# Kernel optimization log

Hardware: AMD Instinct MI355X
Metric: run time of the kernel (lower is better)

The kernel has to match this reference:

```python
import jax, jax.numpy as jnp
import numpy as np

C = 256
R = 8
CR = C // R  # 32


def setup_inputs() -> dict:
    key = jax.random.key(0)
    kx, kq, kk, kv = jax.random.split(key, 4)
    x = jax.random.normal(kx, (4, C, 64, 64), dtype=jnp.float32)
    # 1x1 conv weights, no bias: [out_ch, in_ch]
    Wq = jax.random.normal(kq, (CR, C), dtype=jnp.float32) * (1.0 / np.sqrt(C))
    Wk = jax.random.normal(kk, (CR, C), dtype=jnp.float32) * (1.0 / np.sqrt(C))
    Wv = jax.random.normal(kv, (C, C), dtype=jnp.float32) * (1.0 / np.sqrt(C))
    return {"x": x, "Wq": Wq, "Wk": Wk, "Wv": Wv}


def reference(x, Wq, Wk, Wv):
    B, Cc, H, W = x.shape
    N = H * W
    xf = x.reshape(B, Cc, N)                      # [B, C, N]
    q = jnp.einsum('oc,bcn->bno', Wq, xf)         # [B, N, Cr]
    k = jnp.einsum('oc,bcn->bon', Wk, xf)         # [B, Cr, N]
    v = jnp.einsum('oc,bcn->bon', Wv, xf)         # [B, C, N]
    energy = jnp.einsum('bno,bom->bnm', q, k)     # [B, N, N]
    attn = jax.nn.softmax(energy, axis=-1)
    out = jnp.einsum('bcm,bnm->bcn', v, attn)     # [B, C, N]
    return out.reshape(B, Cc, H, W) + x
```

## Files before the change

kernel.cpp:

```cpp
#include <hip/hip_runtime.h>
#include <stdint.h>
#include <stddef.h>

#define Bn 4
#define Cn 256
#define CRn 32
#define Nn 4096

typedef __attribute__((ext_vector_type(8))) short short8v;
typedef __attribute__((ext_vector_type(4))) float f32x4;

__device__ __forceinline__ unsigned short f2bf(float f) {
  unsigned int u = __float_as_uint(f);
  u += 0x7FFFu + ((u >> 16) & 1u);
  return (unsigned short)(u >> 16);
}

__global__ void __launch_bounds__(256) k_wcast(const float* __restrict__ Wq,
                                               const float* __restrict__ Wk,
                                               const float* __restrict__ Wv,
                                               unsigned short* __restrict__ Wb) {
  int idx = (blockIdx.x * 256 + threadIdx.x) * 4;
  int row = idx >> 8, cc = idx & 255;
  const float* src = (row < 32) ? &Wq[row * 256 + cc]
                   : (row < 64) ? &Wk[(row - 32) * 256 + cc]
                                : &Wv[(row - 64) * 256 + cc];
  float4 f = *reinterpret_cast<const float4*>(src);
  ushort4 o;
  o.x = f2bf(f.x); o.y = f2bf(f.y); o.z = f2bf(f.z); o.w = f2bf(f.w);
  *reinterpret_cast<ushort4*>(&Wb[idx]) = o;
}

__global__ void __launch_bounds__(512) k_proj(const unsigned short* __restrict__ Wb,
                                              const float* __restrict__ x,
                                              unsigned short* __restrict__ Qt,
                                              unsigned short* __restrict__ Kt,
                                              unsigned short* __restrict__ V) {
  __shared__ __align__(16) unsigned char smem[54272];
  unsigned short* xs   = (unsigned short*)smem;
  unsigned short* wbuf = (unsigned short*)(smem + 33792);
  float*          xf   = (float*)(smem + 33792);
  unsigned short* vb   = (unsigned short*)smem;

  const int t  = threadIdx.x;
  const int nt = blockIdx.x, rt = blockIdx.y, b = blockIdx.z;
  const int rbase = rt * 160;
  const int li = t & 15, cr = t >> 4;

  for (int ct = 0; ct < 4; ++ct) {
    if (ct) __syncthreads();
#pragma unroll
    for (int p = 0; p < 2; ++p) {
      int c = cr + (p << 5);
      float4 f = *reinterpret_cast<const float4*>(
          &x[(((size_t)((b << 8) + (ct << 6) + c)) << 12) + (nt << 6) + (li << 2)]);
      xf[c * 65 + (li << 2) + 0] = f.x;
      xf[c * 65 + (li << 2) + 1] = f.y;
      xf[c * 65 + (li << 2) + 2] = f.z;
      xf[c * 65 + (li << 2) + 3] = f.w;
    }
    __syncthreads();
#pragma unroll
    for (int p = 0; p < 2; ++p) {
      int nl = cr + (p << 5);
      int cq = li << 2;
      ushort4 o;
      o.x = f2bf(xf[(cq + 0) * 65 + nl]);
      o.y = f2bf(xf[(cq + 1) * 65 + nl]);
      o.z = f2bf(xf[(cq + 2) * 65 + nl]);
      o.w = f2bf(xf[(cq + 3) * 65 + nl]);
      *reinterpret_cast<ushort4*>(&xs[nl * 264 + (ct << 6) + cq]) = o;
    }
  }
  __syncthreads();

  auto STAGEWB = [&](int ks, int buf) {
#pragma unroll
    for (int r = 0; r < 2; ++r) {
      int idx = (r << 9) + t;
      if (idx < 640) {
        int row = idx >> 2, seg = idx & 3;
        int sseg = seg ^ ((row ^ (row >> 2)) & 3);
        const unsigned short* g =
            Wb + (((size_t)(rbase + row)) << 8) + (ks << 5) + (sseg << 3);
        __builtin_amdgcn_global_load_lds(
            (const __attribute__((address_space(1))) void*)g,
            (__attribute__((address_space(3))) void*)(wbuf + buf * 5120 + idx * 8),
            16, 0, 0);
      }
    }
  };

  STAGEWB(0, 0);
  __syncthreads();

  const int lane = t & 63, w = t >> 6, col = lane & 15, hi = lane >> 4;
  const int nw = w & 3, rh2 = w >> 2;
  f32x4 zero4 = {0.f, 0.f, 0.f, 0.f};
  f32x4 acc[5];
#pragma unroll
  for (int rc = 0; rc < 5; ++rc) acc[rc] = zero4;

#pragma unroll 1
  for (int ks = 0; ks < 8; ++ks) {
    const unsigned short* wB = wbuf + (ks & 1) * 5120;
    if (ks < 7) STAGEWB(ks + 1, (ks & 1) ^ 1);
    short8v af = *reinterpret_cast<const short8v*>(
        &xs[((nw << 4) + col) * 264 + (ks << 5) + (hi << 3)]);
#pragma unroll
    for (int rc = 0; rc < 5; ++rc) {
      int row = rh2 * 80 + (rc << 4) + col;
      int sw = hi ^ ((row ^ (row >> 2)) & 3);
      short8v bf = *reinterpret_cast<const short8v*>(wB + row * 32 + (sw << 3));
      acc[rc] = __builtin_amdgcn_mfma_f32_16x16x32_bf16(af, bf, acc[rc], 0, 0, 0);
    }
    __syncthreads();
  }

  if (rt == 0 && rh2 == 0) {
#pragma unroll
    for (int rc = 0; rc < 2; ++rc)
#pragma unroll
      for (int r = 0; r < 4; ++r) {
        int n = (nt << 6) + (nw << 4) + (hi << 2) + r;
        Qt[(((size_t)((b << 12) + n)) << 5) + (rc << 4) + col] = f2bf(acc[rc][r]);
      }
#pragma unroll
    for (int rc = 2; rc < 4; ++rc)
#pragma unroll
      for (int r = 0; r < 4; ++r) {
        int n = (nt << 6) + (nw << 4) + (hi << 2) + r;
        Kt[(((size_t)((b << 12) + n)) << 5) + ((rc - 2) << 4) + col] = f2bf(acc[rc][r]);
      }
  }

  const int nch = rt ? 160 : 96;
  {
    const int nb = (nw << 4) + (hi << 2);
    const int sub = (rt == 0) ? 64 : 0;
#pragma unroll
    for (int rc = 0; rc < 5; ++rc) {
      int grow_l = rh2 * 80 + (rc << 4) + col;
      int ch_l = grow_l - sub;
      if (ch_l >= 0) {
#pragma unroll
        for (int r = 0; r < 4; ++r)
          vb[ch_l * 72 + nb + r] = f2bf(acc[rc][r]);
      }
    }
  }
  __syncthreads();

  const int cgBase = rt ? 96 : 0;
#pragma unroll
  for (int p = 0; p < 3; ++p) {
    int idx = (p << 9) + t;
    if (idx < nch * 8) {
      int c = idx >> 3, off = idx & 7;
      int offp = off ^ (c & 7);
      int4 dv = *reinterpret_cast<const int4*>(&vb[c * 72 + (offp << 3)]);
      *reinterpret_cast<int4*>(
          &V[(((size_t)((b << 8) + cgBase + c)) << 12) + (nt << 6) + (offp << 3)]) = dv;
    }
  }
}

__global__ void __launch_bounds__(512, 2) k_attn(const unsigned short* __restrict__ Qt,
                                                 const unsigned short* __restrict__ Kt,
                                                 const unsigned short* __restrict__ Vv,
                                                 const float* __restrict__ x,
                                                 float* __restrict__ out) {
  __shared__ unsigned short Qs[64][40];
  __shared__ __align__(16) unsigned short Pt[2][2][64 * 64];
  __shared__ float Sc[2][2][64];
  __shared__ float Mm[2][64], Ll[2][64];
  __shared__ float Ob[4][16][64];

  const int t = threadIdx.x, bx = blockIdx.x;
  const int xcd = bx & 7;
  const int b = xcd >> 1, ch = xcd & 1;
  const int qt = bx >> 3;
  const int lane = t & 63, w = t >> 6, col = lane & 15, hi = lane >> 4;
  const int g = w >> 2, wg = w & 3;
  const int cBase = (ch << 7) + (wg << 5);

  if (t < 256) {
    const int mr = t >> 2, u = t & 3;
    int4 d = *reinterpret_cast<const int4*>(
        Qt + (((size_t)((b << 12) + (qt << 6) + mr)) << 5) + (u << 3));
    *reinterpret_cast<int4*>(&Qs[mr][u << 3]) = d;
  }

  const unsigned short* KtB = Kt + (((size_t)(b << 12)) << 5);
  const unsigned short* VvB = Vv + (((size_t)((b << 8) + cBase)) << 12);

  const int kt0 = g << 5;
  int m0 = kt0 << 6;
  short8v kf[4], vf[4];
#pragma unroll
  for (int mb = 0; mb < 4; ++mb)
    kf[mb] = *reinterpret_cast<const short8v*>(
        KtB + (((size_t)(m0 + (mb << 4) + col)) << 5) + (hi << 3));
#pragma unroll
  for (int ks = 0; ks < 2; ++ks)
#pragma unroll
    for (int cb = 0; cb < 2; ++cb)
      vf[(ks << 1) + cb] = *reinterpret_cast<const short8v*>(
          VvB + (((size_t)((cb << 4) + col)) << 12) + m0 + (ks << 5) + (hi << 3));
  __syncthreads();
  const short8v qf = *reinterpret_cast<const short8v*>(&Qs[(wg << 4) + col][hi << 3]);

  f32x4 zero4 = {0.f, 0.f, 0.f, 0.f};
  f32x4 o_acc[2][4];
#pragma unroll
  for (int cb = 0; cb < 2; ++cb)
#pragma unroll
    for (int nc = 0; nc < 4; ++nc) o_acc[cb][nc] = zero4;
  float m_run = -3e38f, l_run = 0.f;

#pragma unroll 1
  for (int i = 0; i < 32; ++i) {
    const int p = i & 1;
    const int iNext = (i < 31) ? (i + 1) : 31;
    const int mN = (kt0 + iNext) << 6;

    f32x4 s_acc[4];
#pragma unroll
    for (int mb = 0; mb < 4; ++mb)
      s_acc[mb] = __builtin_amdgcn_mfma_f32_16x16x32_bf16(kf[mb], qf, zero4, 0, 0, 0);
#pragma unroll
    for (int mb = 0; mb < 4; ++mb)
      kf[mb] = *reinterpret_cast<const short8v*>(
          KtB + (((size_t)(mN + (mb << 4) + col)) << 5) + (hi << 3));

    float tm = -3e38f;
#pragma unroll
    for (int mb = 0; mb < 4; ++mb)
#pragma unroll
      for (int r = 0; r < 4; ++r) tm = fmaxf(tm, s_acc[mb][r]);
    tm = fmaxf(tm, __shfl_xor(tm, 16));
    tm = fmaxf(tm, __shfl_xor(tm, 32));
    float mn = fmaxf(m_run, tm);
    float sc = __expf(m_run - mn);
    m_run = mn;
    float ps = 0.f;
#pragma unroll
    for (int mb = 0; mb < 4; ++mb)
#pragma unroll
      for (int r = 0; r < 4; ++r) {
        float pv = __expf(s_acc[mb][r] - mn);
        s_acc[mb][r] = pv;
        ps += pv;
      }
    ps += __shfl_xor(ps, 16);
    ps += __shfl_xor(ps, 32);
    l_run = l_run * sc + ps;
    if (hi == 0) Sc[g][p][(wg << 4) + col] = sc;
#pragma unroll
    for (int mb = 0; mb < 4; ++mb) {
      uint2 pk2;
      pk2.x = (unsigned)f2bf(s_acc[mb][0]) | ((unsigned)f2bf(s_acc[mb][1]) << 16);
      pk2.y = (unsigned)f2bf(s_acc[mb][2]) | ((unsigned)f2bf(s_acc[mb][3]) << 16);
      int uu = (mb << 1) + (hi >> 1);
      int up = uu ^ (col & 7);
      *reinterpret_cast<uint2*>(
          &Pt[g][p][(((wg << 4) + col) << 6) + (up << 3) + ((hi & 1) << 2)]) = pk2;
    }

    asm volatile("s_waitcnt lgkmcnt(0)" ::: "memory");
    __builtin_amdgcn_s_barrier();

    float scl[4];
#pragma unroll
    for (int nc = 0; nc < 4; ++nc) scl[nc] = Sc[g][p][(nc << 4) + col];
#pragma unroll
    for (int cb = 0; cb < 2; ++cb)
#pragma unroll
      for (int nc = 0; nc < 4; ++nc) o_acc[cb][nc] *= scl[nc];
#pragma unroll
    for (int ks = 0; ks < 2; ++ks) {
      short8v pb[4];
      int up2 = ((ks << 2) + hi) ^ (col & 7);
#pragma unroll
      for (int nc = 0; nc < 4; ++nc)
        pb[nc] = *reinterpret_cast<const short8v*>(
            &Pt[g][p][(((nc << 4) + col) << 6) + (up2 << 3)]);
#pragma unroll
      for (int cb = 0; cb < 2; ++cb)
#pragma unroll
        for (int nc = 0; nc < 4; ++nc)
          o_acc[cb][nc] = __builtin_amdgcn_mfma_f32_16x16x32_bf16(
              vf[(ks << 1) + cb], pb[nc], o_acc[cb][nc], 0, 0, 0);
    }
#pragma unroll
    for (int ks = 0; ks < 2; ++ks)
#pragma unroll
      for (int cb = 0; cb < 2; ++cb)
        vf[(ks << 1) + cb] = *reinterpret_cast<const short8v*>(
            VvB + (((size_t)((cb << 4) + col)) << 12) + mN + (ks << 5) + (hi << 3));
  }

  if (hi == 0) { Mm[g][(wg << 4) + col] = m_run; Ll[g][(wg << 4) + col] = l_run; }
  __syncthreads();
  float fa[4], fb[4], linv[4];
#pragma unroll
  for (int nc = 0; nc < 4; ++nc) {
    float ma = Mm[0][(nc << 4) + col], mb2 = Mm[1][(nc << 4) + col];
    float mm = fmaxf(ma, mb2);
    float ea = __expf(ma - mm), eb = __expf(mb2 - mm);
    linv[nc] = 1.f / (Ll[0][(nc << 4) + col] * ea + Ll[1][(nc << 4) + col] * eb);
    fa[nc] = ea; fb[nc] = eb;
  }
#pragma unroll
  for (int cb = 0; cb < 2; ++cb) {
    if (g == 1) {
#pragma unroll
      for (int nc = 0; nc < 4; ++nc)
#pragma unroll
        for (int r = 0; r < 4; ++r)
          Ob[wg][(nc << 2) + r][lane] = o_acc[cb][nc][r];
    }
    __syncthreads();
    if (g == 0) {
#pragma unroll
      for (int nc = 0; nc < 4; ++nc)
#pragma unroll
        for (int r = 0; r < 4; ++r) {
          float o = o_acc[cb][nc][r] * fa[nc] + Ob[wg][(nc << 2) + r][lane] * fb[nc];
          int cg = cBase + (cb << 4) + (hi << 2) + r;
          int ng = (qt << 6) + (nc << 4) + col;
          size_t off = (((size_t)((b << 8) + cg)) << 12) + ng;
          out[off] = o * linv[nc] + x[off];
        }
    }
    __syncthreads();
  }
}

extern "C" void kernel_launch(void* const* d_in, const int* in_sizes, int n_in,
                              void* d_out, int out_size, void* d_ws, size_t ws_size,
                              hipStream_t stream) {
  (void)in_sizes; (void)n_in; (void)out_size; (void)ws_size;
  const float* x  = (const float*)d_in[0];
  const float* Wq = (const float*)d_in[1];
  const float* Wk = (const float*)d_in[2];
  const float* Wv = (const float*)d_in[3];
  float* out = (float*)d_out;

  unsigned short* Qt = (unsigned short*)d_ws;
  unsigned short* Kt = Qt + (size_t)Bn * Nn * CRn;
  unsigned short* Vv = Kt + (size_t)Bn * Nn * CRn;
  unsigned short* Wb = Vv + (size_t)Bn * Cn * Nn;

  hipLaunchKernelGGL(k_wcast, dim3(80),        dim3(256), 0, stream, Wq, Wk, Wv, Wb);
  hipLaunchKernelGGL(k_proj,  dim3(64, 2, 4),  dim3(512), 0, stream, Wb, x, Qt, Kt, Vv);
  hipLaunchKernelGGL(k_attn,  dim3(512),       dim3(512), 0, stream, Qt, Kt, Vv, x, out);
}
```

Measured before the change: 175.2 us.

## Retile projection to all output rows per block, skip unchanged softmax rescales

The projection kernel now has each block compute all 320 output rows (Q, K and V) for a 32-column tile, instead of splitting rows across two blocks that each reload the same x tile. This removes the duplicated x loads and transposes, at the cost of twice the weight staging per block and more LDS. In the attention kernel, the running-max update and the output-accumulator rescale are skipped when no lane's max changed. Probability packing now uses the hardware v_cvt_pk_bf16_f32 instruction instead of software rounding.

```diff
diff --git a/kernel.cpp b/kernel.cpp
--- a/kernel.cpp
+++ b/kernel.cpp
@@ -36,56 +36,47 @@
                                               unsigned short* __restrict__ Qt,
                                               unsigned short* __restrict__ Kt,
                                               unsigned short* __restrict__ V) {
-  __shared__ __align__(16) unsigned char smem[54272];
+  __shared__ __align__(16) unsigned char smem[58112];
   unsigned short* xs   = (unsigned short*)smem;
-  unsigned short* wbuf = (unsigned short*)(smem + 33792);
-  float*          xf   = (float*)(smem + 33792);
+  unsigned short* wbuf = (unsigned short*)(smem + 17152);
+  float*          xf   = (float*)(smem + 17152);
   unsigned short* vb   = (unsigned short*)smem;
 
   const int t  = threadIdx.x;
-  const int nt = blockIdx.x, rt = blockIdx.y, b = blockIdx.z;
-  const int rbase = rt * 160;
-  const int li = t & 15, cr = t >> 4;
-
+  const int nt = blockIdx.x, b = blockIdx.y;
+
+  const int cs = t >> 3, nq8 = t & 7;
   for (int ct = 0; ct < 4; ++ct) {
     if (ct) __syncthreads();
-#pragma unroll
-    for (int p = 0; p < 2; ++p) {
-      int c = cr + (p << 5);
-      float4 f = *reinterpret_cast<const float4*>(
-          &x[(((size_t)((b << 8) + (ct << 6) + c)) << 12) + (nt << 6) + (li << 2)]);
-      xf[c * 65 + (li << 2) + 0] = f.x;
-      xf[c * 65 + (li << 2) + 1] = f.y;
-      xf[c * 65 + (li << 2) + 2] = f.z;
-      xf[c * 65 + (li << 2) + 3] = f.w;
-    }
+    float4 f = *reinterpret_cast<const float4*>(
+        &x[(((size_t)((b << 8) + (ct << 6) + cs)) << 12) + (nt << 5) + (nq8 << 2)]);
+    xf[cs * 33 + (nq8 << 2) + 0] = f.x;
+    xf[cs * 33 + (nq8 << 2) + 1] = f.y;
+    xf[cs * 33 + (nq8 << 2) + 2] = f.z;
+    xf[cs * 33 + (nq8 << 2) + 3] = f.w;
     __syncthreads();
-#pragma unroll
-    for (int p = 0; p < 2; ++p) {
-      int nl = cr + (p << 5);
-      int cq = li << 2;
-      ushort4 o;
-      o.x = f2bf(xf[(cq + 0) * 65 + nl]);
-      o.y = f2bf(xf[(cq + 1) * 65 + nl]);
-      o.z = f2bf(xf[(cq + 2) * 65 + nl]);
-      o.w = f2bf(xf[(cq + 3) * 65 + nl]);
-      *reinterpret_cast<ushort4*>(&xs[nl * 264 + (ct << 6) + cq]) = o;
-    }
+    int nl = t >> 4;
+    int cq = (t & 15) << 2;
+    ushort4 o;
+    o.x = f2bf(xf[(cq + 0) * 33 + nl]);
+    o.y = f2bf(xf[(cq + 1) * 33 + nl]);
+    o.z = f2bf(xf[(cq + 2) * 33 + nl]);
+    o.w = f2bf(xf[(cq + 3) * 33 + nl]);
+    *reinterpret_cast<ushort4*>(&xs[nl * 268 + (ct << 6) + cq]) = o;
   }
   __syncthreads();
 
   auto STAGEWB = [&](int ks, int buf) {
 #pragma unroll
-    for (int r = 0; r < 2; ++r) {
+    for (int r = 0; r < 3; ++r) {
       int idx = (r << 9) + t;
-      if (idx < 640) {
+      if (idx < 1280) {
         int row = idx >> 2, seg = idx & 3;
         int sseg = seg ^ ((row ^ (row >> 2)) & 3);
-        const unsigned short* g =
-            Wb + (((size_t)(rbase + row)) << 8) + (ks << 5) + (sseg << 3);
+        const unsigned short* g = Wb + (((size_t)row) << 8) + (ks << 5) + (sseg << 3);
         __builtin_amdgcn_global_load_lds(
             (const __attribute__((address_space(1))) void*)g,
-            (__attribute__((address_space(3))) void*)(wbuf + buf * 5120 + idx * 8),
+            (__attribute__((address_space(3))) void*)(wbuf + buf * 10240 + idx * 8),
             16, 0, 0);
       }
     }
@@ -95,7 +86,7 @@
   __syncthreads();
 
   const int lane = t & 63, w = t >> 6, col = lane & 15, hi = lane >> 4;
-  const int nw = w & 3, rh2 = w >> 2;
+  const int nw = w & 1, rh = w >> 1;
   f32x4 zero4 = {0.f, 0.f, 0.f, 0.f};
   f32x4 acc[5];
 #pragma unroll
@@ -103,13 +94,13 @@
 
 #pragma unroll 1
   for (int ks = 0; ks < 8; ++ks) {
-    const unsigned short* wB = wbuf + (ks & 1) * 5120;
+    const unsigned short* wB = wbuf + (ks & 1) * 10240;
     if (ks < 7) STAGEWB(ks + 1, (ks & 1) ^ 1);
     short8v af = *reinterpret_cast<const short8v*>(
-        &xs[((nw << 4) + col) * 264 + (ks << 5) + (hi << 3)]);
+        &xs[((nw << 4) + col) * 268 + (ks << 5) + (hi << 3)]);
 #pragma unroll
     for (int rc = 0; rc < 5; ++rc) {
-      int row = rh2 * 80 + (rc << 4) + col;
+      int row = rh * 80 + (rc << 4) + col;
       int sw = hi ^ ((row ^ (row >> 2)) & 3);
       short8v bf = *reinterpret_cast<const short8v*>(wB + row * 32 + (sw << 3));
       acc[rc] = __builtin_amdgcn_mfma_f32_16x16x32_bf16(af, bf, acc[rc], 0, 0, 0);
@@ -117,51 +108,45 @@
     __syncthreads();
   }
 
-  if (rt == 0 && rh2 == 0) {
+  if (rh == 0) {
 #pragma unroll
     for (int rc = 0; rc < 2; ++rc)
 #pragma unroll
       for (int r = 0; r < 4; ++r) {
-        int n = (nt << 6) + (nw << 4) + (hi << 2) + r;
+        int n = (nt << 5) + (nw << 4) + (hi << 2) + r;
         Qt[(((size_t)((b << 12) + n)) << 5) + (rc << 4) + col] = f2bf(acc[rc][r]);
       }
 #pragma unroll
     for (int rc = 2; rc < 4; ++rc)
 #pragma unroll
       for (int r = 0; r < 4; ++r) {
-        int n = (nt << 6) + (nw << 4) + (hi << 2) + r;
+        int n = (nt << 5) + (nw << 4) + (hi << 2) + r;
         Kt[(((size_t)((b << 12) + n)) << 5) + ((rc - 2) << 4) + col] = f2bf(acc[rc][r]);
       }
   }
 
-  const int nch = rt ? 160 : 96;
   {
     const int nb = (nw << 4) + (hi << 2);
-    const int sub = (rt == 0) ? 64 : 0;
+    const int rcStart = (rh == 0) ? 4 : 0;
 #pragma unroll
     for (int rc = 0; rc < 5; ++rc) {
-      int grow_l = rh2 * 80 + (rc << 4) + col;
-      int ch_l = grow_l - sub;
-      if (ch_l >= 0) {
-#pragma unroll
-        for (int r = 0; r < 4; ++r)
-          vb[ch_l * 72 + nb + r] = f2bf(acc[rc][r]);
-      }
-    }
-  }
-  __syncthreads();
-
-  const int cgBase = rt ? 96 : 0;
-#pragma unroll
-  for (int p = 0; p < 3; ++p) {
+      if (rc < rcStart) continue;
+      int ch = rh * 80 + (rc << 4) + col - 64;
+#pragma unroll
+      for (int r = 0; r < 4; ++r)
+        vb[ch * 40 + nb + r] = f2bf(acc[rc][r]);
+    }
+  }
+  __syncthreads();
+
+#pragma unroll
+  for (int p = 0; p < 2; ++p) {
     int idx = (p << 9) + t;
-    if (idx < nch * 8) {
-      int c = idx >> 3, off = idx & 7;
-      int offp = off ^ (c & 7);
-      int4 dv = *reinterpret_cast<const int4*>(&vb[c * 72 + (offp << 3)]);
-      *reinterpret_cast<int4*>(
-          &V[(((size_t)((b << 8) + cgBase + c)) << 12) + (nt << 6) + (offp << 3)]) = dv;
-    }
+    int c = idx >> 2, off = idx & 3;
+    int offp = off ^ (c & 3);
+    int4 dv = *reinterpret_cast<const int4*>(&vb[c * 40 + (offp << 3)]);
+    *reinterpret_cast<int4*>(
+        &V[(((size_t)((b << 8) + c)) << 12) + (nt << 5) + (offp << 3)]) = dv;
   }
 }
 
@@ -240,9 +225,15 @@
       for (int r = 0; r < 4; ++r) tm = fmaxf(tm, s_acc[mb][r]);
     tm = fmaxf(tm, __shfl_xor(tm, 16));
     tm = fmaxf(tm, __shfl_xor(tm, 32));
-    float mn = fmaxf(m_run, tm);
-    float sc = __expf(m_run - mn);
-    m_run = mn;
+    float mn, sc;
+    if (__any(tm > m_run)) {
+      mn = fmaxf(m_run, tm);
+      sc = __expf(m_run - mn);
+      m_run = mn;
+    } else {
+      mn = m_run;
+      sc = 1.f;
+    }
     float ps = 0.f;
 #pragma unroll
     for (int mb = 0; mb < 4; ++mb)
@@ -259,8 +250,10 @@
 #pragma unroll
     for (int mb = 0; mb < 4; ++mb) {
       uint2 pk2;
-      pk2.x = (unsigned)f2bf(s_acc[mb][0]) | ((unsigned)f2bf(s_acc[mb][1]) << 16);
-      pk2.y = (unsigned)f2bf(s_acc[mb][2]) | ((unsigned)f2bf(s_acc[mb][3]) << 16);
+      asm("v_cvt_pk_bf16_f32 %0, %1, %2"
+          : "=v"(pk2.x) : "v"(s_acc[mb][0]), "v"(s_acc[mb][1]));
+      asm("v_cvt_pk_bf16_f32 %0, %1, %2"
+          : "=v"(pk2.y) : "v"(s_acc[mb][2]), "v"(s_acc[mb][3]));
       int uu = (mb << 1) + (hi >> 1);
       int up = uu ^ (col & 7);
       *reinterpret_cast<uint2*>(
@@ -273,10 +266,12 @@
     float scl[4];
 #pragma unroll
     for (int nc = 0; nc < 4; ++nc) scl[nc] = Sc[g][p][(nc << 4) + col];
-#pragma unroll
-    for (int cb = 0; cb < 2; ++cb)
-#pragma unroll
-      for (int nc = 0; nc < 4; ++nc) o_acc[cb][nc] *= scl[nc];
+    if (__any((scl[0] != 1.f) | (scl[1] != 1.f) | (scl[2] != 1.f) | (scl[3] != 1.f))) {
+#pragma unroll
+      for (int cb = 0; cb < 2; ++cb)
+#pragma unroll
+        for (int nc = 0; nc < 4; ++nc) o_acc[cb][nc] *= scl[nc];
+    }
 #pragma unroll
     for (int ks = 0; ks < 2; ++ks) {
       short8v pb[4];
@@ -353,6 +348,6 @@
   unsigned short* Wb = Vv + (size_t)Bn * Cn * Nn;
 
   hipLaunchKernelGGL(k_wcast, dim3(80),        dim3(256), 0, stream, Wq, Wk, Wv, Wb);
-  hipLaunchKernelGGL(k_proj,  dim3(64, 2, 4),  dim3(512), 0, stream, Wb, x, Qt, Kt, Vv);
+  hipLaunchKernelGGL(k_proj,  dim3(128, 4),    dim3(512), 0, stream, Wb, x, Qt, Kt, Vv);
   hipLaunchKernelGGL(k_attn,  dim3(512),       dim3(512), 0, stream, Qt, Kt, Vv, x, out);
 }
```

Measured after the change: 178.9 us. 2.1% more time.
